# Optimization experiments

Hardware: AMD Instinct MI355X
Metric: run time of the kernel (lower is better)

Reference implementation:

```python
import jax, jax.numpy as jnp
import numpy as np

TEMPERATURE = 1.0  # module default current_temperature
TOP_K = 2
NUM_EXPERTS = 64
EPS = 1e-10


def setup_inputs() -> dict:
    key = jax.random.key(0)
    k1, k2 = jax.random.split(key)
    x = jax.random.normal(k1, (4, 4096, 2048), dtype=jnp.float32)
    # nn.Linear(d_model, num_experts) weight has shape [num_experts, d_model]
    W_gate = jax.random.normal(k2, (NUM_EXPERTS, 2048), dtype=jnp.float32) * (1.0 / np.sqrt(2048))
    return {"x": x, "W_gate": W_gate}


def reference(x, W_gate):
    # Gate GEMM: [B,S,D] x [E,D] -> [B,S,E]
    logits = jnp.einsum("bsd,ed->bse", x, W_gate)
    scaled = logits / TEMPERATURE
    # Full distribution over experts (for load-balancing loss)
    router_probs = jax.nn.softmax(scaled, axis=-1)
    # Top-k selection over the expert dim, then renormalize via softmax
    top_k_logits, top_k_indices = jax.lax.top_k(scaled, TOP_K)  # [B,S,K]
    top_k_weights = jax.nn.softmax(top_k_logits, axis=-1)
    # Routing stats (no-grad in torch; plain values here)
    entropy = -jnp.sum(router_probs * jnp.log(router_probs + EPS), axis=-1)
    routing_entropy = entropy.mean()
    selection_confidence = top_k_weights[:, :, 0].mean()
    counts = jnp.zeros((NUM_EXPERTS,), dtype=x.dtype).at[top_k_indices.reshape(-1)].add(1.0)
    expert_utilization = counts / (counts.sum() + EPS)
    return (top_k_weights, top_k_indices, router_probs,
            routing_entropy, selection_confidence, expert_utilization)
```

## Files before the change

kernel.cpp:

```cpp
#include <hip/hip_runtime.h>
#include <math.h>

#define NTOK 16384
#define DIM 2048
#define NEXP 64
#define TB 32
#define KG 4
#define CPG 16

#define OFF_W    0
#define OFF_I    32768
#define OFF_P    65536
#define OFF_ENT  1114112
#define OFF_CONF 1114113
#define OFF_UTIL 1114114

typedef short s16x8 __attribute__((ext_vector_type(8)));
typedef float f32x4 __attribute__((ext_vector_type(4)));

__device__ __forceinline__ unsigned short f2bf(float v) {
    unsigned u = __builtin_bit_cast(unsigned, v);
    u = u + 0x7FFFu + ((u >> 16) & 1u);
    return (unsigned short)(u >> 16);
}
__device__ __forceinline__ float bf2f(unsigned short b) {
    return __builtin_bit_cast(float, (unsigned)b << 16);
}

__global__ void router_wsplit(const float* __restrict__ Wg, uint4* __restrict__ wsp,
                              float* __restrict__ out) {
    const int bid = blockIdx.x;
    const int tid = threadIdx.x;
    const int c   = bid >> 2;
    const int gt  = (bid & 3) * 64 + tid;
    if (c == 0 && gt < 66) out[OFF_ENT + gt] = 0.0f;
    const int nt = gt >> 6, l = gt & 63;
    const int e  = 16 * nt + (l & 15);
    const int k0 = 32 * c + 8 * (l >> 4);
    const float* src = Wg + (size_t)e * DIM + k0;
    float4 a = *(const float4*)src;
    float4 b = *(const float4*)(src + 4);
    float v[8] = {a.x, a.y, a.z, a.w, b.x, b.y, b.z, b.w};
    unsigned short H[8], M[8], L[8];
    #pragma unroll
    for (int j = 0; j < 8; ++j) {
        H[j] = f2bf(v[j]);  float r = v[j] - bf2f(H[j]);
        M[j] = f2bf(r);     r = r - bf2f(M[j]);
        L[j] = f2bf(r);
    }
    uint4 ph, pm, pl;
    ph.x = H[0] | ((unsigned)H[1] << 16); ph.y = H[2] | ((unsigned)H[3] << 16);
    ph.z = H[4] | ((unsigned)H[5] << 16); ph.w = H[6] | ((unsigned)H[7] << 16);
    pm.x = M[0] | ((unsigned)M[1] << 16); pm.y = M[2] | ((unsigned)M[3] << 16);
    pm.z = M[4] | ((unsigned)M[5] << 16); pm.w = M[6] | ((unsigned)M[7] << 16);
    pl.x = L[0] | ((unsigned)L[1] << 16); pl.y = L[2] | ((unsigned)L[3] << 16);
    pl.z = L[4] | ((unsigned)L[5] << 16); pl.w = L[6] | ((unsigned)L[7] << 16);
    const int idx = c * 256 + gt;
    wsp[idx]         = ph;
    wsp[16384 + idx] = pm;
    wsp[32768 + idx] = pl;
}

#define LOADW6(W_, i_) {                         \
    W_[0] = wb[(i_) * 256];                      \
    W_[1] = wb[(i_) * 256 + 64];                 \
    W_[2] = wb[(i_) * 256 + 16384];              \
    W_[3] = wb[(i_) * 256 + 16384 + 64];         \
    W_[4] = wb[(i_) * 256 + 32768];              \
    W_[5] = wb[(i_) * 256 + 32768 + 64]; }

#define LOADX4(X_, i_) {                                   \
    X_[0] = *(const float4*)(xb0 + (i_) * 32);             \
    X_[1] = *(const float4*)(xb0 + (i_) * 32 + 4);         \
    X_[2] = *(const float4*)(xb1 + (i_) * 32);             \
    X_[3] = *(const float4*)(xb1 + (i_) * 32 + 4); }

#define CONVA(a0_, a1_) {                                                \
    float xv[8];                                                         \
    xv[0]=a0_.x; xv[1]=a0_.y; xv[2]=a0_.z; xv[3]=a0_.w;                  \
    xv[4]=a1_.x; xv[5]=a1_.y; xv[6]=a1_.z; xv[7]=a1_.w;                  \
    _Pragma("unroll")                                                    \
    for (int j = 0; j < 8; ++j) {                                        \
        unsigned u_  = __builtin_bit_cast(unsigned, xv[j]);              \
        unsigned hb_ = u_ & 0xFFFF0000u;                                 \
        float    r_  = xv[j] - __builtin_bit_cast(float, hb_);           \
        unsigned mb_ = __builtin_bit_cast(unsigned, r_) & 0xFFFF0000u;   \
        float    r2_ = r_ - __builtin_bit_cast(float, mb_);              \
        unsigned lb_ = __builtin_bit_cast(unsigned, r2_);                \
        ah[j] = (short)(hb_ >> 16);                                      \
        am[j] = (short)(mb_ >> 16);                                      \
        al[j] = (short)(lb_ >> 16);                                      \
    } }

#define COMPUTE12(W_, aE_, aO_) {                                        \
    s16x8 b0h_ = __builtin_bit_cast(s16x8, W_[0]);                       \
    s16x8 b1h_ = __builtin_bit_cast(s16x8, W_[1]);                       \
    s16x8 b0m_ = __builtin_bit_cast(s16x8, W_[2]);                       \
    s16x8 b1m_ = __builtin_bit_cast(s16x8, W_[3]);                       \
    s16x8 b0l_ = __builtin_bit_cast(s16x8, W_[4]);                       \
    s16x8 b1l_ = __builtin_bit_cast(s16x8, W_[5]);                       \
    aE_ = __builtin_amdgcn_mfma_f32_16x16x32_bf16(ah, b0h_, aE_, 0, 0, 0); \
    aO_ = __builtin_amdgcn_mfma_f32_16x16x32_bf16(ah, b1h_, aO_, 0, 0, 0); \
    aE_ = __builtin_amdgcn_mfma_f32_16x16x32_bf16(am, b0h_, aE_, 0, 0, 0); \
    aO_ = __builtin_amdgcn_mfma_f32_16x16x32_bf16(am, b1h_, aO_, 0, 0, 0); \
    aE_ = __builtin_amdgcn_mfma_f32_16x16x32_bf16(ah, b0m_, aE_, 0, 0, 0); \
    aO_ = __builtin_amdgcn_mfma_f32_16x16x32_bf16(ah, b1m_, aO_, 0, 0, 0); \
    aE_ = __builtin_amdgcn_mfma_f32_16x16x32_bf16(am, b0m_, aE_, 0, 0, 0); \
    aO_ = __builtin_amdgcn_mfma_f32_16x16x32_bf16(am, b1m_, aO_, 0, 0, 0); \
    aE_ = __builtin_amdgcn_mfma_f32_16x16x32_bf16(ah, b0l_, aE_, 0, 0, 0); \
    aO_ = __builtin_amdgcn_mfma_f32_16x16x32_bf16(ah, b1l_, aO_, 0, 0, 0); \
    aE_ = __builtin_amdgcn_mfma_f32_16x16x32_bf16(al, b0h_, aE_, 0, 0, 0); \
    aO_ = __builtin_amdgcn_mfma_f32_16x16x32_bf16(al, b1h_, aO_, 0, 0, 0); \
    }

__global__ __launch_bounds__(512, 4) void router_main(
    const float* __restrict__ x, const uint4* __restrict__ wq,
    float* __restrict__ out)
{
    __shared__ float lg[TB][NEXP + 1];
    __shared__ float m1s[TB], rss[TB];
    __shared__ float s_ent, s_conf, s_cnt[NEXP];

    const int tid = threadIdx.x;
    const int l   = tid & 63;
    const int w   = tid >> 6;
    const int g   = __builtin_amdgcn_readfirstlane(w >> 1);
    const int np  = __builtin_amdgcn_readfirstlane(w & 1);
    const int qd  = l >> 4;
    const int tr  = l & 15;
    const int t0  = blockIdx.x * TB;

    if (tid == 0) { s_ent = 0.0f; s_conf = 0.0f; }
    if (tid < NEXP) s_cnt[tid] = 0.0f;

    const float* xb0 = x + (size_t)(t0 + tr) * DIM + g * (CPG * 32) + 8 * qd;
    const float* xb1 = xb0 + 16 * DIM;
    const uint4* wb  = wq + (size_t)(g * CPG) * 256 + np * 128 + l;

    f32x4 a00 = (f32x4)(0.0f), a01 = (f32x4)(0.0f);
    f32x4 a10 = (f32x4)(0.0f), a11 = (f32x4)(0.0f);
    s16x8 ah, am, al;
    uint4 wA[6], wB[6];
    float4 xA[4], xB[4];

    LOADW6(wA, 0); LOADX4(xA, 0);
    LOADW6(wB, 1); LOADX4(xB, 1);

    #pragma unroll
    for (int i = 0; i < CPG; i += 2) {
        CONVA(xA[0], xA[1]);  COMPUTE12(wA, a00, a01);
        CONVA(xA[2], xA[3]);  COMPUTE12(wA, a10, a11);
        if (i + 2 < CPG) { LOADW6(wA, i + 2); LOADX4(xA, i + 2); }
        CONVA(xB[0], xB[1]);  COMPUTE12(wB, a00, a01);
        CONVA(xB[2], xB[3]);  COMPUTE12(wB, a10, a11);
        if (i + 3 < CPG) { LOADW6(wB, i + 3); LOADX4(xB, i + 3); }
    }

#define WRROWS(op_) { _Pragma("unroll")                                  \
    for (int r = 0; r < 4; ++r) {                                        \
        lg[4 * qd + r][np * 32 + tr]           op_ a00[r];               \
        lg[4 * qd + r][np * 32 + 16 + tr]      op_ a01[r];               \
        lg[16 + 4 * qd + r][np * 32 + tr]      op_ a10[r];               \
        lg[16 + 4 * qd + r][np * 32 + 16 + tr] op_ a11[r];               \
    } }
    if (g == 3) WRROWS(=);
    __syncthreads();
    if (g == 2) WRROWS(+=);
    __syncthreads();
    if (g == 1) WRROWS(+=);
    __syncthreads();
    if (g == 0) WRROWS(+=);
    __syncthreads();
#undef WRROWS

    if (tid < TB) {
        const int t = tid;
        float m1 = -INFINITY, m2 = -INFINITY;
        int i1 = 0, i2 = 0;
        for (int e = 0; e < NEXP; ++e) {
            float lv = lg[t][e];
            if (lv > m1)      { m2 = m1; i2 = i1; m1 = lv; i1 = e; }
            else if (lv > m2) { m2 = lv; i2 = e; }
        }
        float ssum = 0.0f, tsum = 0.0f;
        for (int e = 0; e < NEXP; ++e) {
            float d = lg[t][e] - m1;
            float ex = __expf(d);
            ssum += ex;
            tsum += d * ex;
        }
        float rs = 1.0f / ssum;
        float H  = logf(ssum) - tsum * rs;
        float e2 = __expf(m2 - m1);
        float rn = 1.0f / (1.0f + e2);
        float w0 = rn, w1v = e2 * rn;
        m1s[t] = m1; rss[t] = rs;

        *(float2*)&out[OFF_W + 2 * (t0 + t)] = make_float2(w0, w1v);
        *(float2*)&out[OFF_I + 2 * (t0 + t)] = make_float2((float)i1, (float)i2);

        atomicAdd(&s_ent,  H);
        atomicAdd(&s_conf, w0);
        atomicAdd(&s_cnt[i1], 1.0f);
        atomicAdd(&s_cnt[i2], 1.0f);
    }
    __syncthreads();

    {
        int t  = tid >> 4;
        int qq = tid & 15;
        float m  = m1s[t];
        float rs = rss[t];
        float4 pr;
        pr.x = __expf(lg[t][4 * qq + 0] - m) * rs;
        pr.y = __expf(lg[t][4 * qq + 1] - m) * rs;
        pr.z = __expf(lg[t][4 * qq + 2] - m) * rs;
        pr.w = __expf(lg[t][4 * qq + 3] - m) * rs;
        *(float4*)&out[OFF_P + (size_t)(t0 + t) * NEXP + 4 * qq] = pr;
    }

    if (tid == 0) {
        atomicAdd(&out[OFF_ENT],  s_ent  * (1.0f / 16384.0f));
        atomicAdd(&out[OFF_CONF], s_conf * (1.0f / 16384.0f));
    }
    if (tid < NEXP)
        atomicAdd(&out[OFF_UTIL + tid], s_cnt[tid] * (1.0f / 32768.0f));
}

extern "C" void kernel_launch(void* const* d_in, const int* in_sizes, int n_in,
                              void* d_out, int out_size, void* d_ws, size_t ws_size,
                              hipStream_t stream) {
    const float* x  = (const float*)d_in[0];
    const float* Wg = (const float*)d_in[1];
    float* out = (float*)d_out;
    (void)in_sizes; (void)n_in; (void)out_size; (void)ws_size;

    router_wsplit<<<dim3(256), dim3(64), 0, stream>>>(Wg, (uint4*)d_ws, out);
    router_main<<<dim3(NTOK / TB), dim3(512), 0, stream>>>(x, (const uint4*)d_ws, out);
}
```

Measured before the change: 238.1 us.

## Split-K gate GEMM with LDS-staged weights and separate wave-parallel softmax kernel

Restructures the router into a split-K GEMM. Each of 256 blocks of 1024 threads loads its K-slice of the bf16-split weights into 96 KB of LDS once and computes 512 tokens by 64 experts. Partial logits go to per-slice workspace buffers, or are atomically accumulated into one buffer when the workspace is too small. A separate post kernel sums the partials and does the top-2, softmax, entropy and stats with wave shuffles, one token per wave. The goal is to cut repeated global weight loads and the serial per-token epilogue, at the cost of extra global traffic for the partial logits and an extra launch.

```diff
diff --git a/kernel.cpp b/kernel.cpp
--- a/kernel.cpp
+++ b/kernel.cpp
@@ -4,9 +4,10 @@
 #define NTOK 16384
 #define DIM 2048
 #define NEXP 64
-#define TB 32
-#define KG 4
-#define CPG 16
+#define KS 8
+#define CPG 8
+#define TPB 512
+#define NTB 32
 
 #define OFF_W    0
 #define OFF_I    32768
@@ -14,6 +15,10 @@
 #define OFF_ENT  1114112
 #define OFF_CONF 1114113
 #define OFF_UTIL 1114114
+
+#define PLG_OFF  196608
+#define PLG_STRIDE 1048576
+#define WS_NEED_STRIDED (786432ull + 33554432ull)
 
 typedef short s16x8 __attribute__((ext_vector_type(8)));
 typedef float f32x4 __attribute__((ext_vector_type(4)));
@@ -61,21 +66,11 @@
     wsp[32768 + idx] = pl;
 }
 
-#define LOADW6(W_, i_) {                         \
-    W_[0] = wb[(i_) * 256];                      \
-    W_[1] = wb[(i_) * 256 + 64];                 \
-    W_[2] = wb[(i_) * 256 + 16384];              \
-    W_[3] = wb[(i_) * 256 + 16384 + 64];         \
-    W_[4] = wb[(i_) * 256 + 32768];              \
-    W_[5] = wb[(i_) * 256 + 32768 + 64]; }
-
-#define LOADX4(X_, i_) {                                   \
-    X_[0] = *(const float4*)(xb0 + (i_) * 32);             \
-    X_[1] = *(const float4*)(xb0 + (i_) * 32 + 4);         \
-    X_[2] = *(const float4*)(xb1 + (i_) * 32);             \
-    X_[3] = *(const float4*)(xb1 + (i_) * 32 + 4); }
-
-#define CONVA(a0_, a1_) {                                                \
+__global__ void router_zero(float* __restrict__ p) {
+    ((float4*)p)[blockIdx.x * 256 + threadIdx.x] = make_float4(0.f, 0.f, 0.f, 0.f);
+}
+
+#define CONVA3(a0_, a1_, AH_, AM_, AL_) {                                \
     float xv[8];                                                         \
     xv[0]=a0_.x; xv[1]=a0_.y; xv[2]=a0_.z; xv[3]=a0_.w;                  \
     xv[4]=a1_.x; xv[5]=a1_.y; xv[6]=a1_.z; xv[7]=a1_.w;                  \
@@ -87,138 +82,167 @@
         unsigned mb_ = __builtin_bit_cast(unsigned, r_) & 0xFFFF0000u;   \
         float    r2_ = r_ - __builtin_bit_cast(float, mb_);              \
         unsigned lb_ = __builtin_bit_cast(unsigned, r2_);                \
-        ah[j] = (short)(hb_ >> 16);                                      \
-        am[j] = (short)(mb_ >> 16);                                      \
-        al[j] = (short)(lb_ >> 16);                                      \
+        AH_[j] = (short)(hb_ >> 16);                                     \
+        AM_[j] = (short)(mb_ >> 16);                                     \
+        AL_[j] = (short)(lb_ >> 16);                                     \
     } }
 
-#define COMPUTE12(W_, aE_, aO_) {                                        \
-    s16x8 b0h_ = __builtin_bit_cast(s16x8, W_[0]);                       \
-    s16x8 b1h_ = __builtin_bit_cast(s16x8, W_[1]);                       \
-    s16x8 b0m_ = __builtin_bit_cast(s16x8, W_[2]);                       \
-    s16x8 b1m_ = __builtin_bit_cast(s16x8, W_[3]);                       \
-    s16x8 b0l_ = __builtin_bit_cast(s16x8, W_[4]);                       \
-    s16x8 b1l_ = __builtin_bit_cast(s16x8, W_[5]);                       \
-    aE_ = __builtin_amdgcn_mfma_f32_16x16x32_bf16(ah, b0h_, aE_, 0, 0, 0); \
-    aO_ = __builtin_amdgcn_mfma_f32_16x16x32_bf16(ah, b1h_, aO_, 0, 0, 0); \
-    aE_ = __builtin_amdgcn_mfma_f32_16x16x32_bf16(am, b0h_, aE_, 0, 0, 0); \
-    aO_ = __builtin_amdgcn_mfma_f32_16x16x32_bf16(am, b1h_, aO_, 0, 0, 0); \
-    aE_ = __builtin_amdgcn_mfma_f32_16x16x32_bf16(ah, b0m_, aE_, 0, 0, 0); \
-    aO_ = __builtin_amdgcn_mfma_f32_16x16x32_bf16(ah, b1m_, aO_, 0, 0, 0); \
-    aE_ = __builtin_amdgcn_mfma_f32_16x16x32_bf16(am, b0m_, aE_, 0, 0, 0); \
-    aO_ = __builtin_amdgcn_mfma_f32_16x16x32_bf16(am, b1m_, aO_, 0, 0, 0); \
-    aE_ = __builtin_amdgcn_mfma_f32_16x16x32_bf16(ah, b0l_, aE_, 0, 0, 0); \
-    aO_ = __builtin_amdgcn_mfma_f32_16x16x32_bf16(ah, b1l_, aO_, 0, 0, 0); \
-    aE_ = __builtin_amdgcn_mfma_f32_16x16x32_bf16(al, b0h_, aE_, 0, 0, 0); \
-    aO_ = __builtin_amdgcn_mfma_f32_16x16x32_bf16(al, b1h_, aO_, 0, 0, 0); \
-    }
-
-__global__ __launch_bounds__(512, 4) void router_main(
+#define MF(A_, B_, C_) __builtin_amdgcn_mfma_f32_16x16x32_bf16(A_, B_, C_, 0, 0, 0)
+#define BC(q_) __builtin_bit_cast(s16x8, q_)
+
+#define PR8(A0_, A1_, Bq_) {                                             \
+    s16x8 b0_ = BC(Bq_[0]), b1_ = BC(Bq_[1]);                            \
+    s16x8 b2_ = BC(Bq_[2]), b3_ = BC(Bq_[3]);                            \
+    a00 = MF(A0_, b0_, a00); a01 = MF(A0_, b1_, a01);                    \
+    a02 = MF(A0_, b2_, a02); a03 = MF(A0_, b3_, a03);                    \
+    a10 = MF(A1_, b0_, a10); a11 = MF(A1_, b1_, a11);                    \
+    a12 = MF(A1_, b2_, a12); a13 = MF(A1_, b3_, a13); }
+
+template<bool STRIDED>
+__global__ __launch_bounds__(1024, 4) void router_main(
     const float* __restrict__ x, const uint4* __restrict__ wq,
-    float* __restrict__ out)
+    float* __restrict__ pl)
 {
-    __shared__ float lg[TB][NEXP + 1];
-    __shared__ float m1s[TB], rss[TB];
-    __shared__ float s_ent, s_conf, s_cnt[NEXP];
+    extern __shared__ uint4 Wl[];
 
     const int tid = threadIdx.x;
     const int l   = tid & 63;
     const int w   = tid >> 6;
-    const int g   = __builtin_amdgcn_readfirstlane(w >> 1);
-    const int np  = __builtin_amdgcn_readfirstlane(w & 1);
+    const int tr  = l & 15;
     const int qd  = l >> 4;
-    const int tr  = l & 15;
-    const int t0  = blockIdx.x * TB;
-
-    if (tid == 0) { s_ent = 0.0f; s_conf = 0.0f; }
-    if (tid < NEXP) s_cnt[tid] = 0.0f;
-
-    const float* xb0 = x + (size_t)(t0 + tr) * DIM + g * (CPG * 32) + 8 * qd;
+    const int kg  = blockIdx.x >> 5;
+    const int tb  = blockIdx.x & 31;
+    const int tw0 = tb * TPB + w * 32;
+
+    #pragma unroll
+    for (int j = 0; j < 6; ++j) {
+        int flat = j * 1024 + tid;
+        int p = flat >> 11, rem = flat & 2047;
+        int c = rem >> 8,  q  = rem & 255;
+        Wl[flat] = wq[p * 16384 + (kg * CPG + c) * 256 + q];
+    }
+    __syncthreads();
+
+    const float* xb0 = x + (size_t)(tw0 + tr) * DIM + kg * (CPG * 32) + 8 * qd;
     const float* xb1 = xb0 + 16 * DIM;
-    const uint4* wb  = wq + (size_t)(g * CPG) * 256 + np * 128 + l;
-
-    f32x4 a00 = (f32x4)(0.0f), a01 = (f32x4)(0.0f);
-    f32x4 a10 = (f32x4)(0.0f), a11 = (f32x4)(0.0f);
-    s16x8 ah, am, al;
-    uint4 wA[6], wB[6];
-    float4 xA[4], xB[4];
-
-    LOADW6(wA, 0); LOADX4(xA, 0);
-    LOADW6(wB, 1); LOADX4(xB, 1);
+
+    f32x4 a00 = (f32x4)(0.f), a01 = (f32x4)(0.f), a02 = (f32x4)(0.f), a03 = (f32x4)(0.f);
+    f32x4 a10 = (f32x4)(0.f), a11 = (f32x4)(0.f), a12 = (f32x4)(0.f), a13 = (f32x4)(0.f);
+    s16x8 ah0, am0, al0, ah1, am1, al1;
+    uint4 bhq[4], bmq[4], blq[4];
+    float4 Xc0, Xc1, Xc2, Xc3, Xn0, Xn1, Xn2, Xn3;
+
+    Xc0 = *(const float4*)(xb0);      Xc1 = *(const float4*)(xb0 + 4);
+    Xc2 = *(const float4*)(xb1);      Xc3 = *(const float4*)(xb1 + 4);
 
     #pragma unroll
-    for (int i = 0; i < CPG; i += 2) {
-        CONVA(xA[0], xA[1]);  COMPUTE12(wA, a00, a01);
-        CONVA(xA[2], xA[3]);  COMPUTE12(wA, a10, a11);
-        if (i + 2 < CPG) { LOADW6(wA, i + 2); LOADX4(xA, i + 2); }
-        CONVA(xB[0], xB[1]);  COMPUTE12(wB, a00, a01);
-        CONVA(xB[2], xB[3]);  COMPUTE12(wB, a10, a11);
-        if (i + 3 < CPG) { LOADW6(wB, i + 3); LOADX4(xB, i + 3); }
-    }
-
-#define WRROWS(op_) { _Pragma("unroll")                                  \
+    for (int c = 0; c < CPG; ++c) {
+        if (c + 1 < CPG) {
+            Xn0 = *(const float4*)(xb0 + (c + 1) * 32);
+            Xn1 = *(const float4*)(xb0 + (c + 1) * 32 + 4);
+            Xn2 = *(const float4*)(xb1 + (c + 1) * 32);
+            Xn3 = *(const float4*)(xb1 + (c + 1) * 32 + 4);
+        }
+        #pragma unroll
+        for (int nt = 0; nt < 4; ++nt) {
+            bhq[nt] = Wl[(0 * CPG + c) * 256 + nt * 64 + l];
+            bmq[nt] = Wl[(1 * CPG + c) * 256 + nt * 64 + l];
+            blq[nt] = Wl[(2 * CPG + c) * 256 + nt * 64 + l];
+        }
+        CONVA3(Xc0, Xc1, ah0, am0, al0);
+        CONVA3(Xc2, Xc3, ah1, am1, al1);
+        PR8(ah0, ah1, bhq);
+        PR8(am0, am1, bhq);
+        PR8(ah0, ah1, bmq);
+        PR8(am0, am1, bmq);
+        PR8(ah0, ah1, blq);
+        PR8(al0, al1, bhq);
+        if (c + 1 < CPG) { Xc0 = Xn0; Xc1 = Xn1; Xc2 = Xn2; Xc3 = Xn3; }
+    }
+
+    float* dst = STRIDED ? (pl + (size_t)kg * PLG_STRIDE) : pl;
+#define STACC(acc_, tt_, nt_) { _Pragma("unroll")                        \
     for (int r = 0; r < 4; ++r) {                                        \
-        lg[4 * qd + r][np * 32 + tr]           op_ a00[r];               \
-        lg[4 * qd + r][np * 32 + 16 + tr]      op_ a01[r];               \
-        lg[16 + 4 * qd + r][np * 32 + tr]      op_ a10[r];               \
-        lg[16 + 4 * qd + r][np * 32 + 16 + tr] op_ a11[r];               \
+        int tok = tw0 + (tt_) * 16 + 4 * qd + r;                         \
+        int ex_ = (nt_) * 16 + tr;                                       \
+        if constexpr (STRIDED) dst[(size_t)tok * 64 + ex_] = acc_[r];    \
+        else atomicAdd(&dst[(size_t)tok * 64 + ex_], acc_[r]);           \
     } }
-    if (g == 3) WRROWS(=);
+    STACC(a00, 0, 0); STACC(a01, 0, 1); STACC(a02, 0, 2); STACC(a03, 0, 3);
+    STACC(a10, 1, 0); STACC(a11, 1, 1); STACC(a12, 1, 2); STACC(a13, 1, 3);
+#undef STACC
+}
+
+__device__ __forceinline__ void merge2(float& m1, int& i1, float& m2, int& i2,
+                                       float om1, int oi1, float om2, int oi2) {
+    bool of = (om1 > m1) || (om1 == m1 && oi1 < i1);
+    float n1, n2; int j1, j2;
+    if (of) {
+        n1 = om1; j1 = oi1;
+        bool s = (m1 > om2) || (m1 == om2 && i1 < oi2);
+        n2 = s ? m1 : om2; j2 = s ? i1 : oi2;
+    } else {
+        n1 = m1; j1 = i1;
+        bool s = (om1 > m2) || (om1 == m2 && oi1 < i2);
+        n2 = s ? om1 : m2; j2 = s ? oi1 : i2;
+    }
+    m1 = n1; i1 = j1; m2 = n2; i2 = j2;
+}
+
+template<int NPART>
+__global__ void router_post(const float* __restrict__ plg, float* __restrict__ out) {
+    __shared__ float s_ent, s_conf, s_cnt[NEXP];
+    const int tid  = threadIdx.x;
+    const int lane = tid & 63;
+    const int wv   = tid >> 6;
+    if (tid == 0) { s_ent = 0.f; s_conf = 0.f; }
+    if (tid < NEXP) s_cnt[tid] = 0.f;
     __syncthreads();
-    if (g == 2) WRROWS(+=);
+
+    const int tb = blockIdx.x * 32 + wv * 8;
+    float entA = 0.f, confA = 0.f;
+
+    for (int k = 0; k < 8; ++k) {
+        const int t = tb + k;
+        float lgv = 0.f;
+        #pragma unroll
+        for (int p = 0; p < NPART; ++p)
+            lgv += plg[(size_t)p * PLG_STRIDE + (size_t)t * 64 + lane];
+
+        float m1 = lgv, m2 = -INFINITY;
+        int   i1 = lane, i2 = 127;
+        #pragma unroll
+        for (int off = 32; off >= 1; off >>= 1) {
+            float om1 = __shfl_xor(m1, off);
+            int   oi1 = __shfl_xor(i1, off);
+            float om2 = __shfl_xor(m2, off);
+            int   oi2 = __shfl_xor(i2, off);
+            merge2(m1, i1, m2, i2, om1, oi1, om2, oi2);
+        }
+        float d  = lgv - m1;
+        float ex = __expf(d);
+        float ss = ex, ts = d * ex;
+        #pragma unroll
+        for (int off = 32; off >= 1; off >>= 1) {
+            ss += __shfl_xor(ss, off);
+            ts += __shfl_xor(ts, off);
+        }
+        float rs = 1.0f / ss;
+        out[OFF_P + (size_t)t * 64 + lane] = ex * rs;
+        if (lane == 0) {
+            float H  = logf(ss) - ts * rs;
+            float e2 = __expf(m2 - m1);
+            float rn = 1.0f / (1.0f + e2);
+            *(float2*)&out[OFF_W + 2 * t] = make_float2(rn, e2 * rn);
+            *(float2*)&out[OFF_I + 2 * t] = make_float2((float)i1, (float)i2);
+            entA  += H;
+            confA += rn;
+            atomicAdd(&s_cnt[i1], 1.0f);
+            atomicAdd(&s_cnt[i2], 1.0f);
+        }
+    }
+    if (lane == 0) { atomicAdd(&s_ent, entA); atomicAdd(&s_conf, confA); }
     __syncthreads();
-    if (g == 1) WRROWS(+=);
-    __syncthreads();
-    if (g == 0) WRROWS(+=);
-    __syncthreads();
-#undef WRROWS
-
-    if (tid < TB) {
-        const int t = tid;
-        float m1 = -INFINITY, m2 = -INFINITY;
-        int i1 = 0, i2 = 0;
-        for (int e = 0; e < NEXP; ++e) {
-            float lv = lg[t][e];
-            if (lv > m1)      { m2 = m1; i2 = i1; m1 = lv; i1 = e; }
-            else if (lv > m2) { m2 = lv; i2 = e; }
-        }
-        float ssum = 0.0f, tsum = 0.0f;
-        for (int e = 0; e < NEXP; ++e) {
-            float d = lg[t][e] - m1;
-            float ex = __expf(d);
-            ssum += ex;
-            tsum += d * ex;
-        }
-        float rs = 1.0f / ssum;
-        float H  = logf(ssum) - tsum * rs;
-        float e2 = __expf(m2 - m1);
-        float rn = 1.0f / (1.0f + e2);
-        float w0 = rn, w1v = e2 * rn;
-        m1s[t] = m1; rss[t] = rs;
-
-        *(float2*)&out[OFF_W + 2 * (t0 + t)] = make_float2(w0, w1v);
-        *(float2*)&out[OFF_I + 2 * (t0 + t)] = make_float2((float)i1, (float)i2);
-
-        atomicAdd(&s_ent,  H);
-        atomicAdd(&s_conf, w0);
-        atomicAdd(&s_cnt[i1], 1.0f);
-        atomicAdd(&s_cnt[i2], 1.0f);
-    }
-    __syncthreads();
-
-    {
-        int t  = tid >> 4;
-        int qq = tid & 15;
-        float m  = m1s[t];
-        float rs = rss[t];
-        float4 pr;
-        pr.x = __expf(lg[t][4 * qq + 0] - m) * rs;
-        pr.y = __expf(lg[t][4 * qq + 1] - m) * rs;
-        pr.z = __expf(lg[t][4 * qq + 2] - m) * rs;
-        pr.w = __expf(lg[t][4 * qq + 3] - m) * rs;
-        *(float4*)&out[OFF_P + (size_t)(t0 + t) * NEXP + 4 * qq] = pr;
-    }
-
     if (tid == 0) {
         atomicAdd(&out[OFF_ENT],  s_ent  * (1.0f / 16384.0f));
         atomicAdd(&out[OFF_CONF], s_conf * (1.0f / 16384.0f));
@@ -233,8 +257,18 @@
     const float* x  = (const float*)d_in[0];
     const float* Wg = (const float*)d_in[1];
     float* out = (float*)d_out;
-    (void)in_sizes; (void)n_in; (void)out_size; (void)ws_size;
+    float* plg = (float*)d_ws + PLG_OFF;
+    (void)in_sizes; (void)n_in; (void)out_size;
 
     router_wsplit<<<dim3(256), dim3(64), 0, stream>>>(Wg, (uint4*)d_ws, out);
-    router_main<<<dim3(NTOK / TB), dim3(512), 0, stream>>>(x, (const uint4*)d_ws, out);
-}
+    if (ws_size >= WS_NEED_STRIDED) {
+        router_main<true><<<dim3(NTB * KS), dim3(1024), 98304, stream>>>(
+            x, (const uint4*)d_ws, plg);
+        router_post<KS><<<dim3(512), dim3(256), 0, stream>>>(plg, out);
+    } else {
+        router_zero<<<dim3(1024), dim3(256), 0, stream>>>(plg);
+        router_main<false><<<dim3(NTB * KS), dim3(1024), 98304, stream>>>(
+            x, (const uint4*)d_ws, plg);
+        router_post<1><<<dim3(512), dim3(256), 0, stream>>>(plg, out);
+    }
+}
```

After: 245.0 us. 2.9% more time.
